# Kernel tuning notes

Measured on AMD Instinct MI355X. Metric: run time of the kernel, lower is better.

## Reference

```python
import jax, jax.numpy as jnp
import numpy as np

F_FILT = 40      # num_filters
K_GABOR = 401    # n_coefficients
K_POOL = 401     # window_length
HOP = 160        # hop_length
SR = 16000
EPS_PCEN = 1e-6
EPS_IN = 1e-5    # nn.InstanceNorm1d default eps
B, T = 8, 160000


def _hz2mel(f):
    return 2595.0 * np.log10(1.0 + f / 700.0)


def _mel2hz(m):
    return 700.0 * (10.0 ** (m / 2595.0) - 1.0)


def setup_inputs() -> dict:
    key = jax.random.key(0)
    x = jax.random.normal(key, (B, 1, T), dtype=jnp.float32)
    # mel-spaced Gabor center frequencies / bandwidths (filter_init_method='mel')
    edges = _mel2hz(np.linspace(_hz2mel(60.0), _hz2mel(7800.0), F_FILT + 2))
    center = edges[1:-1]
    fwhm = np.maximum(edges[2:] - edges[:-2], 1.0)
    eta = 2.0 * np.pi * center / SR                      # rad/sample
    sigma = np.sqrt(2.0 * np.log(2.0)) / (np.pi * fwhm / SR)  # samples
    ones = jnp.ones(F_FILT, jnp.float32)
    return {
        "x": x,
        "gabor_eta": jnp.asarray(eta, jnp.float32),
        "gabor_sigma": jnp.asarray(sigma, jnp.float32),
        "pool_bandwidths": 0.4 * ones,   # GaussianLowPass init
        "pool_bias": ones,               # GaussianLowPass bias init (ones)
        "ema_weights": 0.04 * ones,      # sPCEN smoothing_coefficient, per-channel
        "alpha": 0.96 * ones,
        "delta": 2.0 * ones,
        "root": 0.96 * ones,             # root=compression_factor=0.96
    }


def _conv1d(x, w, stride=1, groups=1):
    # x: (N, C, T), w: (O, C//groups, K); cross-correlation like torch F.conv1d
    return jax.lax.conv_general_dilated(
        x, w, (stride,), "VALID",
        dimension_numbers=("NCH", "OIH", "NCH"),
        feature_group_count=groups)


def _ema_scan(x, s):
    # y_0 = x_0 ; y_t = s*x_t + (1-s)*y_{t-1}  (per-channel s), parallel scan
    s3 = s[None, :, None]
    a = jnp.broadcast_to(1.0 - s3, x.shape)
    b = s3 * x
    a = a.at[:, :, 0].set(0.0)
    b = b.at[:, :, 0].set(x[:, :, 0])
    def comb(c1, c2):
        a1, b1 = c1
        a2, b2 = c2
        return a1 * a2, a2 * b1 + b2
    _, y = jax.lax.associative_scan(comb, (a, b), axis=2)
    return y


def reference(x, gabor_eta, gabor_sigma, pool_bandwidths, pool_bias,
              ema_weights, alpha, delta, root):
    dt = x.dtype
    # --- Gabor complex conv frontend -> |.|^2 ---
    t = jnp.arange(K_GABOR, dtype=dt) - (K_GABOR - 1) / 2.0
    env = jnp.exp(-0.5 * (t[None] / gabor_sigma[:, None]) ** 2) \
          / (jnp.sqrt(2.0 * jnp.pi) * gabor_sigma[:, None])
    phase = gabor_eta[:, None] * t[None]
    kern = jnp.stack([env * jnp.cos(phase), env * jnp.sin(phase)], axis=1)
    kern = kern.reshape(2 * F_FILT, 1, K_GABOR)
    xp = jnp.pad(x, ((0, 0), (0, 0), (K_GABOR - 1, 0)))  # causal pad
    y = _conv1d(xp, kern)                                 # (B, 2F, T)
    y = y.reshape(y.shape[0], F_FILT, 2, y.shape[-1])
    power = y[:, :, 0] ** 2 + y[:, :, 1] ** 2             # |z|^2, (B, F, T)

    # --- sPCEN compression ---
    s = jnp.clip(ema_weights, 0.0, 1.0)
    ema = _ema_scan(power, s)
    a3 = jnp.minimum(alpha, 1.0)[None, :, None]
    inv_r = (1.0 / jnp.maximum(root, 1.0))[None, :, None]
    d3 = delta[None, :, None]
    comp = (power / (EPS_PCEN + ema) ** a3 + d3) ** inv_r - d3 ** inv_r

    # --- Gaussian low-pass depthwise pooling (causal, stride=HOP) ---
    bw = jnp.clip(pool_bandwidths, 2.0 / K_POOL, 0.5)
    tp = jnp.arange(-K_POOL // 2, K_POOL // 2, dtype=dt)  # -201..199, len 401
    den = bw * 0.5 * (K_POOL - 1)
    pk = jnp.exp(-0.5 * (tp[None] / den[:, None]) ** 2).reshape(F_FILT, 1, K_POOL)
    cp = jnp.pad(comp, ((0, 0), (0, 0), (K_POOL - 1, 0)))
    pooled = _conv1d(cp, pk, stride=HOP, groups=F_FILT) + pool_bias[None, :, None]

    # --- InstanceNorm1d (affine=False, biased var, eps=1e-5) ---
    m = pooled.mean(-1, keepdims=True)
    v = pooled.var(-1, keepdims=True)
    return (pooled - m) / jnp.sqrt(v + EPS_IN)
```

## Files before the change

### kernel.cpp

```cpp
#include <hip/hip_runtime.h>
#include <math.h>

#define F_FILT   40
#define K_GABOR  401
#define HOP      160
#define T_LEN    160000
#define B_BATCH  8
#define EPS_PCENF 1e-6f
#define EPS_INF   1e-5f

#define NG       5
#define GF       8
#define NKMAX    13
#define TC       640
#define UW       10
#define NCH1     250
#define NSTG     136
#define PHS      548

#define THREADS  320
#define NWAVES   5
#define RT       10
#define TILE     3200
#define TPC      5
#define CHUNKS   10
#define NPT      20
#define NPOOL_BLK 100
#define KP       208
#define HALOP    200
#define TILEP    1600
#define RINGP    1800

typedef _Float16 h2_t  __attribute__((ext_vector_type(2)));
typedef _Float16 half8 __attribute__((ext_vector_type(8)));
typedef float    f32x4 __attribute__((ext_vector_type(4)));

__device__ __forceinline__ float fdot2(h2_t a, h2_t b, float c) {
    return __builtin_amdgcn_fdot2(a, b, c, false);
}
__device__ __forceinline__ unsigned pk2(float a, float b) {
    return __builtin_bit_cast(unsigned, __builtin_amdgcn_cvt_pkrtz(a, b));
}
__device__ __forceinline__ h2_t bch(unsigned u) {
    return __builtin_bit_cast(h2_t, u);
}
__device__ __forceinline__ float fexp2(float x) { return __builtin_amdgcn_exp2f(x); }
__device__ __forceinline__ float flog2(float x) { return __builtin_amdgcn_logf(x); }

__device__ __forceinline__ void group_span(float sigma0, int& klo, int& nk) {
    const int R = min(200, (int)ceilf(4.5f * sigma0));
    klo = (200 - R) & ~31;
    nk  = ((200 + R - klo) >> 5) + 1;
    if (nk > NKMAX) nk = NKMAX;
}

__global__ __launch_bounds__(256) void leaf_weights(
    const float* __restrict__ eta_g, const float* __restrict__ sigma_g,
    const float* __restrict__ bw_g,
    _Float16* __restrict__ Atab, unsigned* __restrict__ pktab)
{
    const int gi = blockIdx.x;
    const int f0 = gi * GF;
    int klo, nk;
    group_span(sigma_g[f0], klo, nk);

    for (int idx = threadIdx.x; idx < 52 * 16 * 8; idx += 256) {
        const int c8 = idx >> 7;
        const int m  = (idx >> 3) & 15;
        const int i  = idx & 7;
        const int f  = f0 + (m >> 1);
        const int k  = klo + c8 * 8 + i;
        float w = 0.f;
        if (k <= 400) {
            const float sg = sigma_g[f];
            const float t  = (float)(k - 200);
            const float z  = t / sg;
            const float e  = (0.3989422804014327f / sg) * expf(-0.5f * z * z);
            const float ph = eta_g[f] * t;
            w = (m & 1) ? e * sinf(ph) : e * cosf(ph);
        }
        Atab[(size_t)(gi * 52 + c8) * 128 + m * 8 + i] = (_Float16)w;
    }
    for (int idx = threadIdx.x; idx < GF * KP; idx += 256) {
        const int fl = idx / KP, i = idx % KP;
        const int f = f0 + fl;
        const float bw  = fminf(fmaxf(bw_g[f], 2.0f / 401.0f), 0.5f);
        const float den = bw * 0.5f * 400.0f;
        float pp[2];
        for (int j = 0; j < 2; ++j) {
            int k = 2 * i + j;
            float pv = 0.f;
            if (k < K_GABOR) {
                float tp = (float)(k - 201);
                float d = tp / den;
                pv = expf(-0.5f * d * d);
            }
            pp[j] = pv;
        }
        pktab[f * KP + i] = pk2(pp[0], pp[1]);
    }
}

template<int NK>
__device__ __forceinline__ void conv_kloop(
    const uint4* __restrict__ ph4, const uint4* __restrict__ Ap,
    int aBase, int pbase, f32x4* acc)
{
    uint4 F[UW];
#pragma unroll
    for (int u = 0; u < UW; ++u) F[u] = ph4[pbase + 2 * u];
#pragma unroll
    for (int jk = 0; jk < NK; ++jk) {
        const half8 aCur = __builtin_bit_cast(half8, Ap[aBase + jk * 64]);
#pragma unroll
        for (int u = 0; u < UW; ++u) {
            acc[u] = __builtin_amdgcn_mfma_f32_16x16x32_f16(
                aCur, __builtin_bit_cast(half8, F[(2 * jk + u) % UW]), acc[u], 0, 0, 0);
        }
        if (jk + 1 < NK) {
            F[(2 * jk) % UW]     = ph4[pbase + 4 * (jk + 1) + 16];
            F[(2 * jk + 1) % UW] = ph4[pbase + 4 * (jk + 1) + 18];
        }
    }
}

__global__ __launch_bounds__(256) void leaf_conv(
    const float* __restrict__ x,
    const float* __restrict__ sigma_g,
    const _Float16* __restrict__ Atab,
    _Float16* __restrict__ Pall)
{
    __shared__ unsigned ph[8 * PHS];

    const int gi = blockIdx.x % NG;
    const int ch = (blockIdx.x / NG) % NCH1;
    const int b  = blockIdx.x / (NG * NCH1);
    const int f0 = gi * GF;
    const int tid = threadIdx.x;
    const int lane = tid & 63;
    const int w    = tid >> 6;

    const float* __restrict__ xb = x + (size_t)b * T_LEN;
    _Float16* __restrict__ Pb = Pall + (size_t)b * F_FILT * T_LEN;

    int klo, nk;
    group_span(sigma_g[f0], klo, nk);
    const int t0   = ch * TC;
    const int base = t0 + klo - 400;

    if (tid < NSTG) {
        const int g0 = base + 8 * tid;
        float v[15];
        if (g0 >= 0 && g0 + 14 < T_LEN) {
            const float4 a0 = *(const float4*)(xb + g0);
            const float4 a1 = *(const float4*)(xb + g0 + 4);
            const float4 a2 = *(const float4*)(xb + g0 + 8);
            const float4 a3 = *(const float4*)(xb + g0 + 12);
            v[0]=a0.x; v[1]=a0.y; v[2]=a0.z; v[3]=a0.w;
            v[4]=a1.x; v[5]=a1.y; v[6]=a1.z; v[7]=a1.w;
            v[8]=a2.x; v[9]=a2.y; v[10]=a2.z; v[11]=a2.w;
            v[12]=a3.x; v[13]=a3.y; v[14]=a3.z;
        } else {
#pragma unroll
            for (int e = 0; e < 15; ++e) {
                const int gidx = g0 + e;
                v[e] = (gidx >= 0 && gidx < T_LEN) ? xb[gidx] : 0.f;
            }
        }
        unsigned pw[14];
#pragma unroll
        for (int s = 0; s < 14; ++s) pw[s] = pk2(v[s], v[s + 1]);
#pragma unroll
        for (int r = 0; r < 8; ++r) {
            uint4 fr;
            fr.x = pw[r]; fr.y = pw[r + 2]; fr.z = pw[r + 4]; fr.w = pw[r + 6];
            *(uint4*)&ph[r * PHS + 4 * tid] = fr;
        }
    }
    __syncthreads();

    const int n  = lane & 15;
    const int kb = lane >> 4;
    const int q  = n + 8 * kb + 160 * w;
    const int pbase = (q & 7) * (PHS / 4) + (q >> 3);

    f32x4 acc[UW];
#pragma unroll
    for (int u = 0; u < UW; ++u) acc[u] = (f32x4){0.f, 0.f, 0.f, 0.f};

    const uint4* ph4 = (const uint4*)ph;
    const uint4* Ap = (const uint4*)Atab;
    const int aBase = (gi * 52 + kb) * 16 + n;

    switch (nk) {
        case 3:  conv_kloop<3>(ph4, Ap, aBase, pbase, acc); break;
        case 4:  conv_kloop<4>(ph4, Ap, aBase, pbase, acc); break;
        case 5:  conv_kloop<5>(ph4, Ap, aBase, pbase, acc); break;
        case 6:
        case 7:  conv_kloop<7>(ph4, Ap, aBase, pbase, acc); break;
        case 8:
        case 9:  conv_kloop<9>(ph4, Ap, aBase, pbase, acc); break;
        default: conv_kloop<13>(ph4, Ap, aBase, pbase, acc); break;
    }

    const int g  = lane >> 4;
    const int fA = f0 + 2 * g;
#pragma unroll
    for (int u = 0; u < UW; ++u) {
        const int t = t0 + (w * UW + u) * 16 + n;
        const float P0 = acc[u].x * acc[u].x + acc[u].y * acc[u].y;
        const float P1 = acc[u].z * acc[u].z + acc[u].w * acc[u].w;
        Pb[(size_t)fA * T_LEN + t]       = (_Float16)P0;
        Pb[(size_t)(fA + 1) * T_LEN + t] = (_Float16)P1;
    }
}

__global__ __launch_bounds__(THREADS) void leaf_pcen(
    const _Float16* __restrict__ Pall,
    const float* __restrict__ bias_g,
    const float* __restrict__ ema_g,
    const float* __restrict__ alpha_g,
    const float* __restrict__ delta_g,
    const float* __restrict__ root_g,
    const unsigned* __restrict__ pktab,
    float* __restrict__ outp)
{
    __shared__ unsigned ringl[RINGP];
    __shared__ unsigned pkpl[KP];
    __shared__ float pooled[NPOOL_BLK];
    __shared__ float waveV[NWAVES];
    __shared__ float p0Lds;

    const int f     = blockIdx.x % F_FILT;
    const int chunk = (blockIdx.x / F_FILT) % CHUNKS;
    const int b     = blockIdx.x / (F_FILT * CHUNKS);
    const int tid  = threadIdx.x;
    const int lane = tid & 63;
    const int wave = tid >> 6;

    const float sw    = fminf(fmaxf(ema_g[f], 0.0f), 1.0f);
    const float a     = 1.0f - sw;
    const float alpha = fminf(alpha_g[f], 1.0f);
    const float inv_r = 1.0f / fmaxf(root_g[f], 1.0f);
    const float dlt   = delta_g[f];
    const float dpow  = fexp2(inv_r * flog2(dlt));
    const bool  rt1   = (inv_r == 1.0f);

    for (int i = tid; i < RINGP; i += THREADS) ringl[i] = 0u;
    for (int i = tid; i < NPOOL_BLK; i += THREADS) pooled[i] = 0.f;
    if (tid < KP) pkpl[tid] = pktab[f * KP + tid];

    const float a2 = a * a, a4 = a2 * a2, a8 = a4 * a4;
    const float A1  = a8 * a2;
    const float A2  = A1 * A1, A4 = A2 * A2, A8 = A4 * A4;
    const float A16 = A8 * A8, A32 = A16 * A16, A64 = A32 * A32;
    float Al = 1.0f;
    if (lane & 1)  Al *= A1;
    if (lane & 2)  Al *= A2;
    if (lane & 4)  Al *= A4;
    if (lane & 8)  Al *= A8;
    if (lane & 16) Al *= A16;
    if (lane & 32) Al *= A32;

    const unsigned* PU = (const unsigned*)(Pall + ((size_t)b * F_FILT + f) * T_LEN);
    const int tile0 = chunk * TPC;
    const int itStart = (chunk == 0) ? 0 : -1;
    const unsigned P0 = 5u * (unsigned)tid;
    float carry = 0.f;

    unsigned sv[5];
    {
        const int tb = (tile0 + itStart) * 1600 + tid * 5;
#pragma unroll
        for (int q = 0; q < 5; ++q) sv[q] = PU[tb + q];
    }

    for (int it = itStart; it < TPC; ++it) {
        float p[RT];
#pragma unroll
        for (int q = 0; q < 5; ++q) {
            const h2_t hh = bch(sv[q]);
            p[2 * q]     = (float)hh.x;
            p[2 * q + 1] = (float)hh.y;
        }
        {
            const int nt = tile0 + it + 1;
            const int tb = (nt < CHUNKS * TPC ? nt : 0) * 1600 + tid * 5;
#pragma unroll
            for (int q = 0; q < 5; ++q) sv[q] = PU[tb + q];
        }

        float up[RT];
        float uu = 0.f;
#pragma unroll
        for (int r = 0; r < RT; ++r) {
            uu = fmaf(a, uu, sw * p[r]);
            up[r] = uu;
        }
        if (chunk == 0 && it == 0 && tid == 0) p0Lds = p[0];

        const bool doSlide = (it != itStart);
        unsigned tr = 0u;
        if (doSlide && tid < HALOP) tr = ringl[TILEP + tid];

        float v = uu;
        {
            float tv;
            tv = __shfl_up(v, 1);  if (lane >= 1)  v = fmaf(A1,  tv, v);
            tv = __shfl_up(v, 2);  if (lane >= 2)  v = fmaf(A2,  tv, v);
            tv = __shfl_up(v, 4);  if (lane >= 4)  v = fmaf(A4,  tv, v);
            tv = __shfl_up(v, 8);  if (lane >= 8)  v = fmaf(A8,  tv, v);
            tv = __shfl_up(v, 16); if (lane >= 16) v = fmaf(A16, tv, v);
            tv = __shfl_up(v, 32); if (lane >= 32) v = fmaf(A32, tv, v);
        }
        if (lane == 63) waveV[wave] = v;
        __syncthreads();

        if (doSlide && tid < HALOP) ringl[tid] = tr;

        float cw, cc = (chunk == 0 && it == 0) ? p0Lds : carry;
#pragma unroll
        for (int ww = 0; ww < NWAVES; ++ww) {
            if (ww == wave) cw = cc;
            cc = fmaf(A64, cc, waveV[ww]);
        }
        carry = cc;
        float cin;
        {
            float ve = __shfl_up(v, 1);
            if (lane == 0) ve = 0.f;
            cin = fmaf(Al, cw, ve);
        }

        float apr = a;
#pragma unroll
        for (int j = 0; j < 5; ++j) {
            const float e0 = fmaf(apr, cin, up[2 * j]);     apr *= a;
            const float e1 = fmaf(apr, cin, up[2 * j + 1]); apr *= a;
            const float d0 = fexp2(-alpha * flog2(EPS_PCENF + e0));
            const float d1 = fexp2(-alpha * flog2(EPS_PCENF + e1));
            float c0, c1;
            if (rt1) {
                c0 = p[2 * j] * d0;
                c1 = p[2 * j + 1] * d1;
            } else {
                const float q0 = fmaf(p[2 * j],     d0, dlt);
                const float q1 = fmaf(p[2 * j + 1], d1, dlt);
                c0 = fexp2(inv_r * flog2(q0)) - dpow;
                c1 = fexp2(inv_r * flog2(q1)) - dpow;
            }
            ringl[HALOP + P0 + j] = pk2(c0, c1);
        }
        __syncthreads();

        if (it >= 0) {
            const int o = tid >> 4, l = tid & 15;
            float part = 0.f;
#pragma unroll
            for (int t = 0; t < 13; ++t) {
                const int kpp = l + 16 * t;
                part = fdot2(bch(ringl[o * 80 + kpp]), bch(pkpl[kpp]), part);
            }
            part += __shfl_xor(part, 1, 16);
            part += __shfl_xor(part, 2, 16);
            part += __shfl_xor(part, 4, 16);
            part += __shfl_xor(part, 8, 16);
            if (l == 0) pooled[it * NPT + o] += part;
        }
    }
    __syncthreads();

    const float bias = bias_g[f];
    for (int i = tid; i < NPOOL_BLK; i += THREADS)
        outp[((size_t)b * F_FILT + f) * 1000 + (size_t)(tile0 * NPT) + i] = pooled[i] + bias;
}

__global__ __launch_bounds__(256) void leaf_norm(float* __restrict__ out)
{
    const int bf = blockIdx.x;
    float* p = out + (size_t)bf * 1000;
    __shared__ float buf[1000];
    __shared__ float red[4];
    const int tid = threadIdx.x;
    const int lane = tid & 63, wave = tid >> 6;

    float sum = 0.0f;
    for (int i = tid; i < 1000; i += 256) { float v = p[i]; buf[i] = v; sum += v; }
    for (int m = 1; m < 64; m <<= 1) sum += __shfl_xor(sum, m);
    if (lane == 0) red[wave] = sum;
    __syncthreads();
    const float mean = (red[0] + red[1] + red[2] + red[3]) * 0.001f;

    float vs = 0.0f;
    for (int i = tid; i < 1000; i += 256) { float d = buf[i] - mean; vs += d * d; }
    for (int m = 1; m < 64; m <<= 1) vs += __shfl_xor(vs, m);
    __syncthreads();
    if (lane == 0) red[wave] = vs;
    __syncthreads();
    const float var   = (red[0] + red[1] + red[2] + red[3]) * 0.001f;
    const float scale = rsqrtf(var + EPS_INF);
    for (int i = tid; i < 1000; i += 256) p[i] = (buf[i] - mean) * scale;
}

extern "C" void kernel_launch(void* const* d_in, const int* in_sizes, int n_in,
                              void* d_out, int out_size, void* d_ws, size_t ws_size,
                              hipStream_t stream)
{
    const float* x     = (const float*)d_in[0];
    const float* eta   = (const float*)d_in[1];
    const float* sigma = (const float*)d_in[2];
    const float* bw    = (const float*)d_in[3];
    const float* bias  = (const float*)d_in[4];
    const float* emaw  = (const float*)d_in[5];
    const float* alpha = (const float*)d_in[6];
    const float* delta = (const float*)d_in[7];
    const float* root  = (const float*)d_in[8];
    float* outp = (float*)d_out;

    _Float16* Atab  = (_Float16*)d_ws;
    unsigned* pktab = (unsigned*)((char*)d_ws + 133120);
    _Float16* Pall  = (_Float16*)((char*)d_ws + 166400);

    hipLaunchKernelGGL(leaf_weights, dim3(NG), dim3(256), 0, stream,
                       eta, sigma, bw, Atab, pktab);
    hipLaunchKernelGGL(leaf_conv, dim3(B_BATCH * NG * NCH1), dim3(256), 0, stream,
                       x, sigma, Atab, Pall);
    hipLaunchKernelGGL(leaf_pcen, dim3(B_BATCH * F_FILT * CHUNKS), dim3(THREADS), 0, stream,
                       Pall, bias, emaw, alpha, delta, root, pktab, outp);
    hipLaunchKernelGGL(leaf_norm, dim3(B_BATCH * F_FILT), dim3(256), 0, stream, outp);
}
```

Measured before the change: 115.0 us.

## Make PCEN scan wave-independent spans, removing block barriers

Restructures the PCEN/pooling kernel so each wavefront owns an independent 6400-sample span of one (batch, filter) row, with its own LDS ring. The cross-wave carry exchange and both __syncthreads per tile go away, and pooled outputs are written straight to global memory. The cost is more redundant warm-up work per span (one extra tile of halo per wave) and smaller per-wave tiles. The wave-local ring shift also relies on lockstep execution within a wavefront.

```diff
diff --git a/kernel.cpp b/kernel.cpp
--- a/kernel.cpp
+++ b/kernel.cpp
@@ -18,18 +18,17 @@
 #define NSTG     136
 #define PHS      548
 
-#define THREADS  320
-#define NWAVES   5
+#define PC_THREADS 256
+#define PC_NWAVES  4
+#define SPAN     6400
+#define WTILE    640
+#define W_NT     10
+#define NSP      25
 #define RT       10
-#define TILE     3200
-#define TPC      5
-#define CHUNKS   10
-#define NPT      20
-#define NPOOL_BLK 100
 #define KP       208
 #define HALOP    200
-#define TILEP    1600
-#define RINGP    1800
+#define RINGW    520
+#define WSTR     728
 
 typedef _Float16 h2_t  __attribute__((ext_vector_type(2)));
 typedef _Float16 half8 __attribute__((ext_vector_type(8)));
@@ -215,7 +214,7 @@
     }
 }
 
-__global__ __launch_bounds__(THREADS) void leaf_pcen(
+__global__ __launch_bounds__(PC_THREADS) void leaf_pcen(
     const _Float16* __restrict__ Pall,
     const float* __restrict__ bias_g,
     const float* __restrict__ ema_g,
@@ -225,18 +224,18 @@
     const unsigned* __restrict__ pktab,
     float* __restrict__ outp)
 {
-    __shared__ unsigned ringl[RINGP];
-    __shared__ unsigned pkpl[KP];
-    __shared__ float pooled[NPOOL_BLK];
-    __shared__ float waveV[NWAVES];
-    __shared__ float p0Lds;
-
-    const int f     = blockIdx.x % F_FILT;
-    const int chunk = (blockIdx.x / F_FILT) % CHUNKS;
-    const int b     = blockIdx.x / (F_FILT * CHUNKS);
+    __shared__ unsigned lds[PC_NWAVES * WSTR];
+
     const int tid  = threadIdx.x;
     const int lane = tid & 63;
-    const int wave = tid >> 6;
+    const int wv   = tid >> 6;
+    const int wid  = blockIdx.x * PC_NWAVES + wv;
+    const int sp   = wid % NSP;
+    const int bf   = wid / NSP;
+    const int f    = bf % F_FILT;
+
+    unsigned* ring = lds + wv * WSTR;
+    unsigned* pkl  = ring + RINGW;
 
     const float sw    = fminf(fmaxf(ema_g[f], 0.0f), 1.0f);
     const float a     = 1.0f - sw;
@@ -245,10 +244,10 @@
     const float dlt   = delta_g[f];
     const float dpow  = fexp2(inv_r * flog2(dlt));
     const bool  rt1   = (inv_r == 1.0f);
-
-    for (int i = tid; i < RINGP; i += THREADS) ringl[i] = 0u;
-    for (int i = tid; i < NPOOL_BLK; i += THREADS) pooled[i] = 0.f;
-    if (tid < KP) pkpl[tid] = pktab[f * KP + tid];
+    const float bias  = bias_g[f];
+
+    for (int i = lane; i < KP; i += 64) pkl[i] = pktab[f * KP + i];
+    for (int i = lane; i < HALOP; i += 64) ring[i] = 0u;
 
     const float a2 = a * a, a4 = a2 * a2, a8 = a4 * a4;
     const float A1  = a8 * a2;
@@ -262,20 +261,19 @@
     if (lane & 16) Al *= A16;
     if (lane & 32) Al *= A32;
 
-    const unsigned* PU = (const unsigned*)(Pall + ((size_t)b * F_FILT + f) * T_LEN);
-    const int tile0 = chunk * TPC;
-    const int itStart = (chunk == 0) ? 0 : -1;
-    const unsigned P0 = 5u * (unsigned)tid;
+    const unsigned* PU = (const unsigned*)(Pall + (size_t)bf * T_LEN);
+    const int wbase = sp * (SPAN / 2);
+    const int itStart = (sp == 0) ? 0 : -1;
     float carry = 0.f;
 
     unsigned sv[5];
     {
-        const int tb = (tile0 + itStart) * 1600 + tid * 5;
+        const int tb = wbase + itStart * 320 + lane * 5;
 #pragma unroll
         for (int q = 0; q < 5; ++q) sv[q] = PU[tb + q];
     }
 
-    for (int it = itStart; it < TPC; ++it) {
+    for (int it = itStart; it < W_NT; ++it) {
         float p[RT];
 #pragma unroll
         for (int q = 0; q < 5; ++q) {
@@ -284,8 +282,8 @@
             p[2 * q + 1] = (float)hh.y;
         }
         {
-            const int nt = tile0 + it + 1;
-            const int tb = (nt < CHUNKS * TPC ? nt : 0) * 1600 + tid * 5;
+            const int nt = it + 1;
+            const int tb = wbase + (nt < W_NT ? nt : 0) * 320 + lane * 5;
 #pragma unroll
             for (int q = 0; q < 5; ++q) sv[q] = PU[tb + q];
         }
@@ -297,11 +295,9 @@
             uu = fmaf(a, uu, sw * p[r]);
             up[r] = uu;
         }
-        if (chunk == 0 && it == 0 && tid == 0) p0Lds = p[0];
-
-        const bool doSlide = (it != itStart);
-        unsigned tr = 0u;
-        if (doSlide && tid < HALOP) tr = ringl[TILEP + tid];
+
+        float cc = carry;
+        if (sp == 0 && it == 0) cc = __shfl(p[0], 0);
 
         float v = uu;
         {
@@ -313,24 +309,14 @@
             tv = __shfl_up(v, 16); if (lane >= 16) v = fmaf(A16, tv, v);
             tv = __shfl_up(v, 32); if (lane >= 32) v = fmaf(A32, tv, v);
         }
-        if (lane == 63) waveV[wave] = v;
-        __syncthreads();
-
-        if (doSlide && tid < HALOP) ringl[tid] = tr;
-
-        float cw, cc = (chunk == 0 && it == 0) ? p0Lds : carry;
-#pragma unroll
-        for (int ww = 0; ww < NWAVES; ++ww) {
-            if (ww == wave) cw = cc;
-            cc = fmaf(A64, cc, waveV[ww]);
-        }
-        carry = cc;
+        const float vlast = __shfl(v, 63);
         float cin;
         {
             float ve = __shfl_up(v, 1);
             if (lane == 0) ve = 0.f;
-            cin = fmaf(Al, cw, ve);
-        }
+            cin = fmaf(Al, cc, ve);
+        }
+        carry = fmaf(A64, cc, vlast);
 
         float apr = a;
 #pragma unroll
@@ -349,30 +335,27 @@
                 c0 = fexp2(inv_r * flog2(q0)) - dpow;
                 c1 = fexp2(inv_r * flog2(q1)) - dpow;
             }
-            ringl[HALOP + P0 + j] = pk2(c0, c1);
-        }
-        __syncthreads();
+            ring[HALOP + lane * 5 + j] = pk2(c0, c1);
+        }
 
         if (it >= 0) {
-            const int o = tid >> 4, l = tid & 15;
+            const int o = lane >> 4, l = lane & 15;
             float part = 0.f;
 #pragma unroll
             for (int t = 0; t < 13; ++t) {
                 const int kpp = l + 16 * t;
-                part = fdot2(bch(ringl[o * 80 + kpp]), bch(pkpl[kpp]), part);
+                part = fdot2(bch(ring[o * 80 + kpp]), bch(pkl[kpp]), part);
             }
             part += __shfl_xor(part, 1, 16);
             part += __shfl_xor(part, 2, 16);
             part += __shfl_xor(part, 4, 16);
             part += __shfl_xor(part, 8, 16);
-            if (l == 0) pooled[it * NPT + o] += part;
-        }
-    }
-    __syncthreads();
-
-    const float bias = bias_g[f];
-    for (int i = tid; i < NPOOL_BLK; i += THREADS)
-        outp[((size_t)b * F_FILT + f) * 1000 + (size_t)(tile0 * NPT) + i] = pooled[i] + bias;
+            if (l == 0)
+                outp[(size_t)bf * 1000 + sp * (W_NT * 4) + it * 4 + o] = part + bias;
+        }
+
+        for (int i = lane; i < HALOP; i += 64) ring[i] = ring[320 + i];
+    }
 }
 
 __global__ __launch_bounds__(256) void leaf_norm(float* __restrict__ out)
@@ -425,7 +408,7 @@
                        eta, sigma, bw, Atab, pktab);
     hipLaunchKernelGGL(leaf_conv, dim3(B_BATCH * NG * NCH1), dim3(256), 0, stream,
                        x, sigma, Atab, Pall);
-    hipLaunchKernelGGL(leaf_pcen, dim3(B_BATCH * F_FILT * CHUNKS), dim3(THREADS), 0, stream,
-                       Pall, bias, emaw, alpha, delta, root, pktab, outp);
+    hipLaunchKernelGGL(leaf_pcen, dim3(B_BATCH * F_FILT * NSP / PC_NWAVES), dim3(PC_THREADS),
+                       0, stream, Pall, bias, emaw, alpha, delta, root, pktab, outp);
     hipLaunchKernelGGL(leaf_norm, dim3(B_BATCH * F_FILT), dim3(256), 0, stream, outp);
 }
```

Result: faster. 105.0 us (-8.7%).
